# Optimization experiments

Hardware: AMD Instinct MI355X
Metric: run time of the kernel (lower is better)

The kernel has to match this reference:

```python
import jax, jax.numpy as jnp
import numpy as np

B, F, H, E = 16384, 128, 64, 16


def setup_inputs() -> dict:
    key = jax.random.key(0)
    k_x, k_w1, k_b1, k_w2, k_b2 = jax.random.split(key, 5)
    # Per-feature stacked params: Linear(1,H) -> W1 [F,H], b1 [F,H];
    # Linear(H,E) -> W2 [F,E,H], b2 [F,E]. Scaled like torch default init.
    x = jax.random.normal(k_x, (B, F), dtype=jnp.float32)
    W1 = jax.random.uniform(k_w1, (F, H), jnp.float32, -1.0, 1.0)  # bound = 1/sqrt(in=1)
    b1 = jax.random.uniform(k_b1, (F, H), jnp.float32, -1.0, 1.0)
    bnd = 1.0 / np.sqrt(H)
    W2 = jax.random.uniform(k_w2, (F, E, H), jnp.float32, -bnd, bnd)
    b2 = jax.random.uniform(k_b2, (F, E), jnp.float32, -bnd, bnd)
    return {"x": x, "W1": W1, "b1": b1, "W2": W2, "b2": b2}


def reference(x, W1, b1, W2, b2) -> jnp.ndarray:
    # h[b,f,h] = relu(x[b,f] * W1[f,h] + b1[f,h])   (Linear(1,H) is a scalar-vector product)
    h = jax.nn.relu(x[:, :, None] * W1[None, :, :] + b1[None, :, :])  # [B,F,H]
    # emb[b,f,e] = sum_h h[b,f,h] * W2[f,e,h] + b2[f,e]
    emb = jnp.einsum("bfh,feh->bfe", h, W2) + b2[None, :, :]  # [B,F,E]
    # concat per-feature embeddings along last dim -> [B, F*E]
    return emb.reshape(x.shape[0], -1)
```

## Files before the change

kernel.cpp:

```cpp
#include <hip/hip_runtime.h>


#define F_   128
#define H_   64
#define E_   16
#define NROW 65
#define GRS  32
#define FPB  4
#define RPI  16
#define ITERS 8
#define BPB  (RPI * ITERS)
#define THREADS 256

typedef float vf4 __attribute__((ext_vector_type(4)));

__global__ __launch_bounds__(64) void build_tables(
    const float* __restrict__ W1, const float* __restrict__ B1,
    const float* __restrict__ W2, const float* __restrict__ B2,
    float* __restrict__ tbl, float* __restrict__ bps)
{
    const int f = blockIdx.x;
    const int e = blockIdx.y;
    const int h = threadIdx.x;

    __shared__ float ts_raw[H_];
    __shared__ float ts_sorted[H_];
    __shared__ float scS[H_];
    __shared__ float scT[H_];

    const float w1 = W1[f * H_ + h];
    const float bb = B1[f * H_ + h];
    const bool  slope = (w1 != 0.0f);
    const float t   = slope ? (-bb / w1) : __builtin_inff();
    const float sgn = slope ? (w1 > 0.0f ? 1.0f : -1.0f) : 0.0f;
    const bool act0 = (w1 < 0.0f) || (!slope && bb > 0.0f);

    ts_raw[h] = t;
    __syncthreads();
    int rank = 0;
    #pragma unroll
    for (int j = 0; j < H_; ++j) {
        float tj = ts_raw[j];
        rank += (tj < t || (tj == t && j < h)) ? 1 : 0;
    }
    ts_sorted[rank] = t;
    __syncthreads();
    if (e == 0) bps[f * H_ + h] = ts_sorted[h];

    const float w2 = W2[(f * E_ + e) * H_ + h];
    const float dS = sgn * w1 * w2;
    const float dT = sgn * bb * w2;
    float bS = act0 ? w1 * w2 : 0.0f;
    float bT = act0 ? bb * w2 : 0.0f;
    #pragma unroll
    for (int d = 32; d; d >>= 1) { bS += __shfl_xor(bS, d); bT += __shfl_xor(bT, d); }

    scS[rank] = dS; scT[rank] = dT;
    __syncthreads();
    float vS = scS[h], vT = scT[h];
    #pragma unroll
    for (int d = 1; d < 64; d <<= 1) {
        float uS = __shfl_up(vS, (unsigned)d);
        float uT = __shfl_up(vT, (unsigned)d);
        if (h >= d) { vS += uS; vT += uT; }
    }
    const float b2v = B2[f * E_ + e];
    float* row = tbl + ((size_t)f * NROW + (h + 1)) * GRS;
    row[e]      = bS + vS;
    row[E_ + e] = bT + vT + b2v;
    if (h == 0) {
        float* r0 = tbl + (size_t)f * NROW * GRS;
        r0[e]      = bS;
        r0[E_ + e] = bT + b2v;
    }
}

__global__ __launch_bounds__(THREADS, 4) void embed_main(
    const float* __restrict__ x, const float* __restrict__ tbl,
    const float* __restrict__ bps, float* __restrict__ out)
{
    const int tid = threadIdx.x;
    const int f0  = blockIdx.x * FPB;

    const int   eq   = tid & 3;
    const int   fl   = (tid >> 2) & 3;
    const int   rloc = tid >> 4;
    const int   f    = f0 + fl;
    const int bbase  = blockIdx.y * BPB;

    float xs[ITERS];
    #pragma unroll
    for (int it = 0; it < ITERS; ++it)
        xs[it] = x[(size_t)(bbase + it * RPI + rloc) * F_ + f];

    float4 bp[4];
    #pragma unroll
    for (int i = 0; i < 4; ++i)
        bp[i] = *(const float4*)(bps + (size_t)f * H_ + eq * 16 + 4 * i);

    const float* ftbl = tbl + (size_t)f * NROW * GRS;

    #pragma unroll
    for (int it = 0; it < ITERS; ++it) {
        const int   b  = bbase + it * RPI + rloc;
        const float xv = xs[it];
        int c = 0;
        #pragma unroll
        for (int i = 0; i < 4; ++i) {
            c += (bp[i].x <= xv) ? 1 : 0;
            c += (bp[i].y <= xv) ? 1 : 0;
            c += (bp[i].z <= xv) ? 1 : 0;
            c += (bp[i].w <= xv) ? 1 : 0;
        }
        c += __shfl_xor(c, 1);
        c += __shfl_xor(c, 2);
        const float* row = ftbl + (size_t)c * GRS + eq * 4;
        float4 S = *(const float4*)(row);
        float4 T = *(const float4*)(row + E_);
        vf4 o;
        o.x = fmaf(S.x, xv, T.x);
        o.y = fmaf(S.y, xv, T.y);
        o.z = fmaf(S.z, xv, T.z);
        o.w = fmaf(S.w, xv, T.w);
        vf4* op = (vf4*)(out + (size_t)b * (F_ * E_) + f * E_ + eq * 4);
        *op = o;
    }
}

extern "C" void kernel_launch(void* const* d_in, const int* in_sizes, int n_in,
                              void* d_out, int out_size, void* d_ws, size_t ws_size,
                              hipStream_t stream) {
    const float* x  = (const float*)d_in[0];
    const float* W1 = (const float*)d_in[1];
    const float* b1 = (const float*)d_in[2];
    const float* W2 = (const float*)d_in[3];
    const float* b2 = (const float*)d_in[4];
    float* out = (float*)d_out;
    const int B = in_sizes[0] / F_;

    float* tbl = (float*)d_ws;
    float* bps = tbl + (size_t)F_ * NROW * GRS;

    build_tables<<<dim3(F_, E_), 64, 0, stream>>>(W1, b1, W2, b2, tbl, bps);
    dim3 grid(F_ / FPB, B / BPB);
    embed_main<<<grid, THREADS, 0, stream>>>(x, tbl, bps, out);
}
```

Baseline: 165.5 us.

## Remap embed kernel so each block writes full contiguous output rows

Each block now handles 16 batch rows across all 128 features, with each thread covering two features (f and f+64). A wave's stores become contiguous 4KB row segments, replacing the earlier scattered 64-byte-per-feature segments across many rows. The grid becomes 1D over the batch. In exchange, each block loads breakpoints for all features, x loads become strided per thread, and register pressure rises from keeping two sets of breakpoints and 32 x values.

```diff
diff --git a/kernel.cpp b/kernel.cpp
--- a/kernel.cpp
+++ b/kernel.cpp
@@ -6,10 +6,7 @@
 #define E_   16
 #define NROW 65
 #define GRS  32
-#define FPB  4
-#define RPI  16
-#define ITERS 8
-#define BPB  (RPI * ITERS)
+#define RPB  16
 #define THREADS 256
 
 typedef float vf4 __attribute__((ext_vector_type(4)));
@@ -80,50 +77,68 @@
     const float* __restrict__ bps, float* __restrict__ out)
 {
     const int tid = threadIdx.x;
-    const int f0  = blockIdx.x * FPB;
+    const int el  = tid & 3;
+    const int fq  = tid >> 2;
+    const int fA  = fq;
+    const int fB  = fq + 64;
+    const int r0  = blockIdx.x * RPB;
 
-    const int   eq   = tid & 3;
-    const int   fl   = (tid >> 2) & 3;
-    const int   rloc = tid >> 4;
-    const int   f    = f0 + fl;
-    const int bbase  = blockIdx.y * BPB;
+    float xsA[RPB], xsB[RPB];
+    #pragma unroll
+    for (int i = 0; i < RPB; ++i) {
+        xsA[i] = x[(size_t)(r0 + i) * F_ + fA];
+        xsB[i] = x[(size_t)(r0 + i) * F_ + fB];
+    }
 
-    float xs[ITERS];
+    float4 bpA[4], bpB[4];
     #pragma unroll
-    for (int it = 0; it < ITERS; ++it)
-        xs[it] = x[(size_t)(bbase + it * RPI + rloc) * F_ + f];
+    for (int i = 0; i < 4; ++i) {
+        bpA[i] = *(const float4*)(bps + (size_t)fA * H_ + el * 16 + 4 * i);
+        bpB[i] = *(const float4*)(bps + (size_t)fB * H_ + el * 16 + 4 * i);
+    }
 
-    float4 bp[4];
-    #pragma unroll
-    for (int i = 0; i < 4; ++i)
-        bp[i] = *(const float4*)(bps + (size_t)f * H_ + eq * 16 + 4 * i);
-
-    const float* ftbl = tbl + (size_t)f * NROW * GRS;
+    const float* tA = tbl + (size_t)fA * NROW * GRS;
+    const float* tB = tbl + (size_t)fB * NROW * GRS;
 
     #pragma unroll
-    for (int it = 0; it < ITERS; ++it) {
-        const int   b  = bbase + it * RPI + rloc;
-        const float xv = xs[it];
-        int c = 0;
+    for (int i = 0; i < RPB; ++i) {
+        const float xa = xsA[i];
+        const float xb = xsB[i];
+        int ca = 0, cb = 0;
         #pragma unroll
-        for (int i = 0; i < 4; ++i) {
-            c += (bp[i].x <= xv) ? 1 : 0;
-            c += (bp[i].y <= xv) ? 1 : 0;
-            c += (bp[i].z <= xv) ? 1 : 0;
-            c += (bp[i].w <= xv) ? 1 : 0;
+        for (int j = 0; j < 4; ++j) {
+            ca += (bpA[j].x <= xa) ? 1 : 0;
+            ca += (bpA[j].y <= xa) ? 1 : 0;
+            ca += (bpA[j].z <= xa) ? 1 : 0;
+            ca += (bpA[j].w <= xa) ? 1 : 0;
+            cb += (bpB[j].x <= xb) ? 1 : 0;
+            cb += (bpB[j].y <= xb) ? 1 : 0;
+            cb += (bpB[j].z <= xb) ? 1 : 0;
+            cb += (bpB[j].w <= xb) ? 1 : 0;
         }
-        c += __shfl_xor(c, 1);
-        c += __shfl_xor(c, 2);
-        const float* row = ftbl + (size_t)c * GRS + eq * 4;
-        float4 S = *(const float4*)(row);
-        float4 T = *(const float4*)(row + E_);
-        vf4 o;
-        o.x = fmaf(S.x, xv, T.x);
-        o.y = fmaf(S.y, xv, T.y);
-        o.z = fmaf(S.z, xv, T.z);
-        o.w = fmaf(S.w, xv, T.w);
-        vf4* op = (vf4*)(out + (size_t)b * (F_ * E_) + f * E_ + eq * 4);
-        *op = o;
+        ca += __shfl_xor(ca, 1);  cb += __shfl_xor(cb, 1);
+        ca += __shfl_xor(ca, 2);  cb += __shfl_xor(cb, 2);
+
+        const float* rowA = tA + (size_t)ca * GRS + el * 4;
+        const float* rowB = tB + (size_t)cb * GRS + el * 4;
+        float4 SA = *(const float4*)(rowA);
+        float4 TA = *(const float4*)(rowA + E_);
+        float4 SB = *(const float4*)(rowB);
+        float4 TB = *(const float4*)(rowB + E_);
+
+        vf4 oA, oB;
+        oA.x = fmaf(SA.x, xa, TA.x);
+        oA.y = fmaf(SA.y, xa, TA.y);
+        oA.z = fmaf(SA.z, xa, TA.z);
+        oA.w = fmaf(SA.w, xa, TA.w);
+        oB.x = fmaf(SB.x, xb, TB.x);
+        oB.y = fmaf(SB.y, xb, TB.y);
+        oB.z = fmaf(SB.z, xb, TB.z);
+        oB.w = fmaf(SB.w, xb, TB.w);
+
+        float* orow = out + (size_t)(r0 + i) * (F_ * E_);
+        *(vf4*)(orow + tid * 4)            = oA;
+        *(vf4*)(orow + 1024 + tid * 4)     = oB;
     }
 }
 
@@ -142,6 +157,5 @@
     float* bps = tbl + (size_t)F_ * NROW * GRS;
 
     build_tables<<<dim3(F_, E_), 64, 0, stream>>>(W1, b1, W2, b2, tbl, bps);
-    dim3 grid(F_ / FPB, B / BPB);
-    embed_main<<<grid, THREADS, 0, stream>>>(x, tbl, bps, out);
+    embed_main<<<B / RPB, THREADS, 0, stream>>>(x, tbl, bps, out);
 }
```

New measurement: 171.1 us. 3.3% more time.
